# Kernel tuning notes

Hardware: AMD Instinct MI355X
Metric: run time of the kernel (lower is better)

## Reference

```python
import jax, jax.numpy as jnp
import numpy as np

N_CYCLES = 20000  # number of cycles in the cycle basis (segments)


def setup_inputs() -> dict:
    key = jax.random.key(0)
    k1, k2, k3, k4, k5 = jax.random.split(key, 5)
    B, NB, E = 256, 50000, 160000  # batch, n_branches, total cycle-basis entries
    c = jax.random.normal(k1, (B, NB), dtype=jnp.float32)
    s = jax.random.normal(k2, (B, NB), dtype=jnp.float32)
    # signs are +/-1
    cysigns = jnp.where(jax.random.uniform(k4, (E,)) < 0.5, -1.0, 1.0).astype(jnp.float32)
    cyinds = jax.random.randint(k3, (E,), 0, NB, dtype=jnp.int32)
    # from_value_rowids requires nondecreasing row ids
    cyrows = jnp.sort(jax.random.randint(k5, (E,), 0, N_CYCLES, dtype=jnp.int32))
    return {"c": c, "s": s, "cysigns": cysigns, "cyinds": cyinds, "cyrows": cyrows}


def reference(c, s, cysigns, cyinds, cyrows):
    # gather branch vars per cycle-basis entry: [B, E]
    cg = jnp.take(c, cyinds, axis=1)
    sg = cysigns * jnp.take(s, cyinds, axis=1)
    # tf.math.angle(tf.complex(rc, rs)) == atan2(imag, real)
    ang = jnp.arctan2(sg, cg)  # [B, E]
    # ragged per-cycle sum == segment_sum over the entry axis -> [N_CYCLES, B]
    v_kvl = jax.ops.segment_sum(ang.T, cyrows, num_segments=N_CYCLES)
    # scalar KVL violation
    return jnp.mean(jnp.abs(v_kvl))
```

## Files before the change

### kernel.cpp

```cpp
#include <hip/hip_runtime.h>

#define NB     50000
#define NB4    12500
#define BATCH  256
#define NCYC   20000
#define QSCALE  (127.0f / 3.14159265358979f)
#define DQSCALE (3.14159265358979f / 127.0f)

__device__ __forceinline__ float fast_atan2f(float y, float x) {
    const float ax = __builtin_fabsf(x);
    const float ay = __builtin_fabsf(y);
    const float mx = fmaxf(ax, ay);
    const float mn = fminf(ax, ay);
    const float t  = mn * __builtin_amdgcn_rcpf(mx);
    const float t2 = t * t;
    float p = fmaf(t2, fmaf(t2, fmaf(t2, fmaf(t2,
                  0.0208351f, -0.0851330f), 0.1801410f), -0.3302995f),
                  0.9998660f);
    p *= t;
    p = (ay > ax) ? (1.57079632679489662f - p) : p;
    p = (x < 0.0f) ? (3.14159265358979324f - p) : p;
    return copysignf(p, y);
}

__global__ __launch_bounds__(256) void theta_k(
        const float4* __restrict__ c4, const float4* __restrict__ s4,
        signed char* __restrict__ th) {
    __shared__ signed char t[64][68];
    const int u    = threadIdx.x;
    const int col4 = u & 15;
    const int brow = u >> 4;
    const int x4   = blockIdx.x * 16 + col4;
    const int bb   = blockIdx.y * 64;

    if (x4 < NB4) {
        #pragma unroll
        for (int j = 0; j < 4; ++j) {
            const int bl = brow + 16 * j;
            const float4 vc = c4[(size_t)(bb + bl) * NB4 + x4];
            const float4 vs = s4[(size_t)(bb + bl) * NB4 + x4];
            char4 q;
            q.x = (signed char)__float2int_rn(fast_atan2f(vs.x, vc.x) * QSCALE);
            q.y = (signed char)__float2int_rn(fast_atan2f(vs.y, vc.y) * QSCALE);
            q.z = (signed char)__float2int_rn(fast_atan2f(vs.z, vc.z) * QSCALE);
            q.w = (signed char)__float2int_rn(fast_atan2f(vs.w, vc.w) * QSCALE);
            *reinterpret_cast<char4*>(&t[bl][4 * col4]) = q;
        }
    }
    __syncthreads();
    const int g   = u & 15;
    const int nb0 = u >> 4;
    #pragma unroll
    for (int j = 0; j < 4; ++j) {
        const int nbl = nb0 + 16 * j;
        const int nb  = blockIdx.x * 64 + nbl;
        if (nb < NB) {
            char4 v;
            v.x = t[4 * g + 0][nbl];
            v.y = t[4 * g + 1][nbl];
            v.z = t[4 * g + 2][nbl];
            v.w = t[4 * g + 3][nbl];
            *reinterpret_cast<char4*>(&th[(size_t)nb * BATCH + bb + 4 * g]) = v;
        }
    }
}

__global__ __launch_bounds__(256) void kvl_main_k(
        const signed char* __restrict__ th,
        const float* __restrict__ signs, const int* __restrict__ inds,
        const int* __restrict__ rows, int E,
        float* __restrict__ partials) {
    __shared__ int bnd[5];
    const int tid = threadIdx.x;
    const int r0  = blockIdx.x * 4;
    if (tid < 5) {
        const int target = r0 + tid;
        int lo = 0, hi = E;
        while (lo < hi) { const int m = (lo + hi) >> 1; if (rows[m] < target) lo = m + 1; else hi = m; }
        bnd[tid] = lo;
    }
    __syncthreads();
    const int wave  = tid >> 6;
    const int lane  = tid & 63;
    const int start = bnd[wave];
    const int end   = bnd[wave + 1];

    float a0 = 0.f, a1 = 0.f, a2 = 0.f, a3 = 0.f;
    int e = start;
    for (; e + 2 <= end; e += 2) {
        const int   i0 = inds[e],  i1 = inds[e + 1];
        const float g0 = signs[e] * DQSCALE, g1 = signs[e + 1] * DQSCALE;
        const unsigned int u0 = *reinterpret_cast<const unsigned int*>(&th[(size_t)i0 * BATCH + lane * 4]);
        const unsigned int u1 = *reinterpret_cast<const unsigned int*>(&th[(size_t)i1 * BATCH + lane * 4]);
        a0 += g0 * (float)(signed char)(u0      ) + g1 * (float)(signed char)(u1      );
        a1 += g0 * (float)(signed char)(u0 >>  8) + g1 * (float)(signed char)(u1 >>  8);
        a2 += g0 * (float)(signed char)(u0 >> 16) + g1 * (float)(signed char)(u1 >> 16);
        a3 += g0 * (float)(signed char)(u0 >> 24) + g1 * (float)(signed char)(u1 >> 24);
    }
    if (e < end) {
        const float g0 = signs[e] * DQSCALE;
        const unsigned int u0 = *reinterpret_cast<const unsigned int*>(&th[(size_t)inds[e] * BATCH + lane * 4]);
        a0 += g0 * (float)(signed char)(u0      );
        a1 += g0 * (float)(signed char)(u0 >>  8);
        a2 += g0 * (float)(signed char)(u0 >> 16);
        a3 += g0 * (float)(signed char)(u0 >> 24);
    }
    float v = fabsf(a0) + fabsf(a1) + fabsf(a2) + fabsf(a3);
    #pragma unroll
    for (int off = 32; off > 0; off >>= 1)
        v += __shfl_down(v, off, 64);
    if (lane == 0) partials[r0 + wave] = v;
}

__global__ __launch_bounds__(1024) void reduce_k(
        const float* __restrict__ partials, float* __restrict__ out) {
    const int tid = threadIdx.x;
    float v = 0.f;
    for (int i = tid; i < NCYC; i += 1024) v += partials[i];
    #pragma unroll
    for (int off = 32; off > 0; off >>= 1)
        v += __shfl_down(v, off, 64);
    __shared__ float wsum[16];
    if ((tid & 63) == 0) wsum[tid >> 6] = v;
    __syncthreads();
    if (tid == 0) {
        float t = 0.f;
        #pragma unroll
        for (int w = 0; w < 16; ++w) t += wsum[w];
        out[0] = t * (1.0f / ((float)NCYC * (float)BATCH));
    }
}

__global__ void zero_out_k(float* out) { if (threadIdx.x == 0) out[0] = 0.0f; }

__global__ __launch_bounds__(256) void kvl_fallback_k(
        const float* __restrict__ c, const float* __restrict__ s,
        const float* __restrict__ signs, const int* __restrict__ inds,
        const int* __restrict__ rows, int E, float* __restrict__ out) {
    const int r = blockIdx.x;
    int lo = 0, hi = E;
    while (lo < hi) { const int m = (lo + hi) >> 1; if (rows[m] < r) lo = m + 1; else hi = m; }
    const int start = lo;
    hi = E;
    while (lo < hi) { const int m = (lo + hi) >> 1; if (rows[m] <= r) lo = m + 1; else hi = m; }
    const int end = lo;
    const int tid = threadIdx.x;
    float acc = 0.f;
    for (int e = start; e < end; ++e) {
        const int idx = inds[e];
        const float sg = signs[e];
        acc += atan2f(sg * s[(size_t)tid * NB + idx], c[(size_t)tid * NB + idx]);
    }
    float v = fabsf(acc);
    #pragma unroll
    for (int off = 32; off > 0; off >>= 1)
        v += __shfl_down(v, off, 64);
    __shared__ float wsum[4];
    if ((tid & 63) == 0) wsum[tid >> 6] = v;
    __syncthreads();
    if (tid == 0)
        atomicAdd(out, (wsum[0] + wsum[1] + wsum[2] + wsum[3]) *
                       (1.0f / ((float)NCYC * (float)BATCH)));
}

extern "C" void kernel_launch(void* const* d_in, const int* in_sizes, int n_in,
                              void* d_out, int out_size, void* d_ws, size_t ws_size,
                              hipStream_t stream) {
    const float* c       = (const float*)d_in[0];
    const float* s       = (const float*)d_in[1];
    const float* cysigns = (const float*)d_in[2];
    const int*   cyinds  = (const int*)d_in[3];
    const int*   cyrows  = (const int*)d_in[4];
    const int    E       = in_sizes[2];
    float* out = (float*)d_out;

    const size_t th_bytes = (size_t)NB * BATCH;
    const size_t need = th_bytes + (size_t)NCYC * sizeof(float);
    if (ws_size >= need) {
        signed char* th = (signed char*)d_ws;
        float* partials = (float*)(th + th_bytes);

        dim3 tg((NB4 + 15) / 16, BATCH / 64);
        theta_k<<<tg, 256, 0, stream>>>((const float4*)c, (const float4*)s, th);
        kvl_main_k<<<NCYC / 4, 256, 0, stream>>>(th, cysigns, cyinds, cyrows, E, partials);
        reduce_k<<<1, 1024, 0, stream>>>(partials, out);
    } else {
        zero_out_k<<<1, 64, 0, stream>>>(out);
        kvl_fallback_k<<<NCYC, 256, 0, stream>>>(c, s, cysigns, cyinds, cyrows, E, out);
    }
}
```

Baseline: 166.2 us.

## Fuse theta, KVL gather and reduction into one cooperative kernel with grid sync

Merges the three kernels (theta quantize/transpose, per-cycle gather-sum, final reduce) into one cooperative launch of 782 blocks that uses a grid-wide sync between phases. Row boundaries are precomputed once per cycle into a workspace array, so the per-block binary searches go away. The final reduction becomes a per-block atomicAdd. This removes two launch gaps, but it caps the grid at 782 blocks, so each block handles four batch tiles in the theta phase, and it adds the cost of the grid barrier.

```diff
diff --git a/kernel.cpp b/kernel.cpp
--- a/kernel.cpp
+++ b/kernel.cpp
@@ -1,11 +1,16 @@
 #include <hip/hip_runtime.h>
+#include <hip/hip_cooperative_groups.h>
+
+namespace cg = cooperative_groups;
 
 #define NB     50000
 #define NB4    12500
 #define BATCH  256
 #define NCYC   20000
+#define GRID_F 782
 #define QSCALE  (127.0f / 3.14159265358979f)
 #define DQSCALE (3.14159265358979f / 127.0f)
+#define OUTSCALE (1.0f / ((float)NCYC * (float)BATCH))
 
 __device__ __forceinline__ float fast_atan2f(float y, float x) {
     const float ax = __builtin_fabsf(x);
@@ -23,112 +28,103 @@
     return copysignf(p, y);
 }
 
-__global__ __launch_bounds__(256) void theta_k(
+__global__ __launch_bounds__(256, 4) void fused_k(
         const float4* __restrict__ c4, const float4* __restrict__ s4,
-        signed char* __restrict__ th) {
+        signed char* __restrict__ th, int* __restrict__ row_start,
+        const float* __restrict__ signs, const int* __restrict__ inds,
+        const int* __restrict__ rows, int E, float* __restrict__ out) {
     __shared__ signed char t[64][68];
-    const int u    = threadIdx.x;
+    __shared__ float wsum[4];
+    const int u = threadIdx.x;
+
+    if (blockIdx.x == 0 && u == 0) out[0] = 0.0f;
+
+    {
+        const int g = blockIdx.x * 256 + u;
+        if (g <= NCYC) {
+            int lo = 0, hi = E;
+            while (lo < hi) { const int m = (lo + hi) >> 1; if (rows[m] < g) lo = m + 1; else hi = m; }
+            row_start[g] = lo;
+        }
+    }
+
     const int col4 = u & 15;
     const int brow = u >> 4;
     const int x4   = blockIdx.x * 16 + col4;
-    const int bb   = blockIdx.y * 64;
-
-    if (x4 < NB4) {
+    #pragma unroll
+    for (int by = 0; by < 4; ++by) {
+        const int bb = by * 64;
+        if (x4 < NB4) {
+            #pragma unroll
+            for (int j = 0; j < 4; ++j) {
+                const int bl = brow + 16 * j;
+                const float4 vc = c4[(size_t)(bb + bl) * NB4 + x4];
+                const float4 vs = s4[(size_t)(bb + bl) * NB4 + x4];
+                char4 q;
+                q.x = (signed char)__float2int_rn(fast_atan2f(vs.x, vc.x) * QSCALE);
+                q.y = (signed char)__float2int_rn(fast_atan2f(vs.y, vc.y) * QSCALE);
+                q.z = (signed char)__float2int_rn(fast_atan2f(vs.z, vc.z) * QSCALE);
+                q.w = (signed char)__float2int_rn(fast_atan2f(vs.w, vc.w) * QSCALE);
+                *reinterpret_cast<char4*>(&t[bl][4 * col4]) = q;
+            }
+        }
+        __syncthreads();
+        const int g2  = u & 15;
+        const int nb0 = u >> 4;
         #pragma unroll
         for (int j = 0; j < 4; ++j) {
-            const int bl = brow + 16 * j;
-            const float4 vc = c4[(size_t)(bb + bl) * NB4 + x4];
-            const float4 vs = s4[(size_t)(bb + bl) * NB4 + x4];
-            char4 q;
-            q.x = (signed char)__float2int_rn(fast_atan2f(vs.x, vc.x) * QSCALE);
-            q.y = (signed char)__float2int_rn(fast_atan2f(vs.y, vc.y) * QSCALE);
-            q.z = (signed char)__float2int_rn(fast_atan2f(vs.z, vc.z) * QSCALE);
-            q.w = (signed char)__float2int_rn(fast_atan2f(vs.w, vc.w) * QSCALE);
-            *reinterpret_cast<char4*>(&t[bl][4 * col4]) = q;
+            const int nbl = nb0 + 16 * j;
+            const int nb  = blockIdx.x * 64 + nbl;
+            if (nb < NB) {
+                char4 v;
+                v.x = t[4 * g2 + 0][nbl];
+                v.y = t[4 * g2 + 1][nbl];
+                v.z = t[4 * g2 + 2][nbl];
+                v.w = t[4 * g2 + 3][nbl];
+                *reinterpret_cast<char4*>(&th[(size_t)nb * BATCH + bb + 4 * g2]) = v;
+            }
         }
+        __syncthreads();
     }
-    __syncthreads();
-    const int g   = u & 15;
-    const int nb0 = u >> 4;
-    #pragma unroll
-    for (int j = 0; j < 4; ++j) {
-        const int nbl = nb0 + 16 * j;
-        const int nb  = blockIdx.x * 64 + nbl;
-        if (nb < NB) {
-            char4 v;
-            v.x = t[4 * g + 0][nbl];
-            v.y = t[4 * g + 1][nbl];
-            v.z = t[4 * g + 2][nbl];
-            v.w = t[4 * g + 3][nbl];
-            *reinterpret_cast<char4*>(&th[(size_t)nb * BATCH + bb + 4 * g]) = v;
+
+    cg::this_grid().sync();
+
+    const int wave = u >> 6;
+    const int lane = u & 63;
+    const int w0   = blockIdx.x * 4 + wave;
+    float acc = 0.f;
+    for (int r = w0; r < NCYC; r += 4 * GRID_F) {
+        const int start = row_start[r];
+        const int end   = row_start[r + 1];
+        float a0 = 0.f, a1 = 0.f, a2 = 0.f, a3 = 0.f;
+        int e = start;
+        for (; e + 2 <= end; e += 2) {
+            const int   i0 = inds[e],  i1 = inds[e + 1];
+            const float g0 = signs[e] * DQSCALE, g1 = signs[e + 1] * DQSCALE;
+            const unsigned int u0 = *reinterpret_cast<const unsigned int*>(&th[(size_t)i0 * BATCH + lane * 4]);
+            const unsigned int u1 = *reinterpret_cast<const unsigned int*>(&th[(size_t)i1 * BATCH + lane * 4]);
+            a0 += g0 * (float)(signed char)(u0      ) + g1 * (float)(signed char)(u1      );
+            a1 += g0 * (float)(signed char)(u0 >>  8) + g1 * (float)(signed char)(u1 >>  8);
+            a2 += g0 * (float)(signed char)(u0 >> 16) + g1 * (float)(signed char)(u1 >> 16);
+            a3 += g0 * (float)(signed char)(u0 >> 24) + g1 * (float)(signed char)(u1 >> 24);
         }
+        if (e < end) {
+            const float g0 = signs[e] * DQSCALE;
+            const unsigned int u0 = *reinterpret_cast<const unsigned int*>(&th[(size_t)inds[e] * BATCH + lane * 4]);
+            a0 += g0 * (float)(signed char)(u0      );
+            a1 += g0 * (float)(signed char)(u0 >>  8);
+            a2 += g0 * (float)(signed char)(u0 >> 16);
+            a3 += g0 * (float)(signed char)(u0 >> 24);
+        }
+        acc += fabsf(a0) + fabsf(a1) + fabsf(a2) + fabsf(a3);
     }
-}
-
-__global__ __launch_bounds__(256) void kvl_main_k(
-        const signed char* __restrict__ th,
-        const float* __restrict__ signs, const int* __restrict__ inds,
-        const int* __restrict__ rows, int E,
-        float* __restrict__ partials) {
-    __shared__ int bnd[5];
-    const int tid = threadIdx.x;
-    const int r0  = blockIdx.x * 4;
-    if (tid < 5) {
-        const int target = r0 + tid;
-        int lo = 0, hi = E;
-        while (lo < hi) { const int m = (lo + hi) >> 1; if (rows[m] < target) lo = m + 1; else hi = m; }
-        bnd[tid] = lo;
-    }
-    __syncthreads();
-    const int wave  = tid >> 6;
-    const int lane  = tid & 63;
-    const int start = bnd[wave];
-    const int end   = bnd[wave + 1];
-
-    float a0 = 0.f, a1 = 0.f, a2 = 0.f, a3 = 0.f;
-    int e = start;
-    for (; e + 2 <= end; e += 2) {
-        const int   i0 = inds[e],  i1 = inds[e + 1];
-        const float g0 = signs[e] * DQSCALE, g1 = signs[e + 1] * DQSCALE;
-        const unsigned int u0 = *reinterpret_cast<const unsigned int*>(&th[(size_t)i0 * BATCH + lane * 4]);
-        const unsigned int u1 = *reinterpret_cast<const unsigned int*>(&th[(size_t)i1 * BATCH + lane * 4]);
-        a0 += g0 * (float)(signed char)(u0      ) + g1 * (float)(signed char)(u1      );
-        a1 += g0 * (float)(signed char)(u0 >>  8) + g1 * (float)(signed char)(u1 >>  8);
-        a2 += g0 * (float)(signed char)(u0 >> 16) + g1 * (float)(signed char)(u1 >> 16);
-        a3 += g0 * (float)(signed char)(u0 >> 24) + g1 * (float)(signed char)(u1 >> 24);
-    }
-    if (e < end) {
-        const float g0 = signs[e] * DQSCALE;
-        const unsigned int u0 = *reinterpret_cast<const unsigned int*>(&th[(size_t)inds[e] * BATCH + lane * 4]);
-        a0 += g0 * (float)(signed char)(u0      );
-        a1 += g0 * (float)(signed char)(u0 >>  8);
-        a2 += g0 * (float)(signed char)(u0 >> 16);
-        a3 += g0 * (float)(signed char)(u0 >> 24);
-    }
-    float v = fabsf(a0) + fabsf(a1) + fabsf(a2) + fabsf(a3);
     #pragma unroll
     for (int off = 32; off > 0; off >>= 1)
-        v += __shfl_down(v, off, 64);
-    if (lane == 0) partials[r0 + wave] = v;
-}
-
-__global__ __launch_bounds__(1024) void reduce_k(
-        const float* __restrict__ partials, float* __restrict__ out) {
-    const int tid = threadIdx.x;
-    float v = 0.f;
-    for (int i = tid; i < NCYC; i += 1024) v += partials[i];
-    #pragma unroll
-    for (int off = 32; off > 0; off >>= 1)
-        v += __shfl_down(v, off, 64);
-    __shared__ float wsum[16];
-    if ((tid & 63) == 0) wsum[tid >> 6] = v;
+        acc += __shfl_down(acc, off, 64);
+    if (lane == 0) wsum[wave] = acc;
     __syncthreads();
-    if (tid == 0) {
-        float t = 0.f;
-        #pragma unroll
-        for (int w = 0; w < 16; ++w) t += wsum[w];
-        out[0] = t * (1.0f / ((float)NCYC * (float)BATCH));
-    }
+    if (u == 0)
+        atomicAdd(out, (wsum[0] + wsum[1] + wsum[2] + wsum[3]) * OUTSCALE);
 }
 
 __global__ void zero_out_k(float* out) { if (threadIdx.x == 0) out[0] = 0.0f; }
@@ -171,19 +167,22 @@
     const float* cysigns = (const float*)d_in[2];
     const int*   cyinds  = (const int*)d_in[3];
     const int*   cyrows  = (const int*)d_in[4];
-    const int    E       = in_sizes[2];
+    int          E       = in_sizes[2];
     float* out = (float*)d_out;
 
     const size_t th_bytes = (size_t)NB * BATCH;
-    const size_t need = th_bytes + (size_t)NCYC * sizeof(float);
+    const size_t need = th_bytes + (size_t)(NCYC + 1) * sizeof(int);
     if (ws_size >= need) {
         signed char* th = (signed char*)d_ws;
-        float* partials = (float*)(th + th_bytes);
+        int* row_start  = (int*)(th + th_bytes);
 
-        dim3 tg((NB4 + 15) / 16, BATCH / 64);
-        theta_k<<<tg, 256, 0, stream>>>((const float4*)c, (const float4*)s, th);
-        kvl_main_k<<<NCYC / 4, 256, 0, stream>>>(th, cysigns, cyinds, cyrows, E, partials);
-        reduce_k<<<1, 1024, 0, stream>>>(partials, out);
+        const float4* c4 = (const float4*)c;
+        const float4* s4 = (const float4*)s;
+        void* args[] = {(void*)&c4, (void*)&s4, (void*)&th, (void*)&row_start,
+                        (void*)&cysigns, (void*)&cyinds, (void*)&cyrows,
+                        (void*)&E, (void*)&out};
+        hipLaunchCooperativeKernel((void*)fused_k, dim3(GRID_F), dim3(256),
+                                   args, 0, stream);
     } else {
         zero_out_k<<<1, 64, 0, stream>>>(out);
         kvl_fallback_k<<<NCYC, 256, 0, stream>>>(c, s, cysigns, cyinds, cyrows, E, out);
```

Result: slower. 258.3 us (+55.4%).

## Fuse final reduction into KVL kernel and precompute row boundaries in theta kernel

Applied to the files above, without the earlier changes.

Moves the per-cycle binary searches for segment boundaries into the theta kernel, where the blockIdx.y==0 blocks write a row_start array. The KVL kernel now reads its boundaries directly and reduces to one partial per block. The last block to finish, found with an atomic ticket counter, does the final reduction, which removes the separate single-block reduce launch. This cuts one kernel launch and the serial tail, at the cost of extra work in some theta blocks and an atomic plus fences per block.

```diff
diff --git a/kernel.cpp b/kernel.cpp
--- a/kernel.cpp
+++ b/kernel.cpp
@@ -6,6 +6,7 @@
 #define NCYC   20000
 #define QSCALE  (127.0f / 3.14159265358979f)
 #define DQSCALE (3.14159265358979f / 127.0f)
+#define OUTSCALE (1.0f / ((float)NCYC * (float)BATCH))
 
 __device__ __forceinline__ float fast_atan2f(float y, float x) {
     const float ax = __builtin_fabsf(x);
@@ -25,9 +26,22 @@
 
 __global__ __launch_bounds__(256) void theta_k(
         const float4* __restrict__ c4, const float4* __restrict__ s4,
-        signed char* __restrict__ th) {
+        signed char* __restrict__ th, int* __restrict__ row_start,
+        const int* __restrict__ rows, int E, int* __restrict__ counter) {
     __shared__ signed char t[64][68];
-    const int u    = threadIdx.x;
+    const int u = threadIdx.x;
+
+    if (blockIdx.x == 0 && blockIdx.y == 0 && u == 0) *counter = 0;
+
+    if (blockIdx.y == 0) {
+        const int g = blockIdx.x * 256 + u;
+        if (g <= NCYC) {
+            int lo = 0, hi = E;
+            while (lo < hi) { const int m = (lo + hi) >> 1; if (rows[m] < g) lo = m + 1; else hi = m; }
+            row_start[g] = lo;
+        }
+    }
+
     const int col4 = u & 15;
     const int brow = u >> 4;
     const int x4   = blockIdx.x * 16 + col4;
@@ -65,25 +79,20 @@
     }
 }
 
-__global__ __launch_bounds__(256) void kvl_main_k(
+__global__ __launch_bounds__(256) void kvl2_k(
         const signed char* __restrict__ th,
         const float* __restrict__ signs, const int* __restrict__ inds,
-        const int* __restrict__ rows, int E,
-        float* __restrict__ partials) {
-    __shared__ int bnd[5];
-    const int tid = threadIdx.x;
-    const int r0  = blockIdx.x * 4;
-    if (tid < 5) {
-        const int target = r0 + tid;
-        int lo = 0, hi = E;
-        while (lo < hi) { const int m = (lo + hi) >> 1; if (rows[m] < target) lo = m + 1; else hi = m; }
-        bnd[tid] = lo;
-    }
-    __syncthreads();
-    const int wave  = tid >> 6;
-    const int lane  = tid & 63;
-    const int start = bnd[wave];
-    const int end   = bnd[wave + 1];
+        const int* __restrict__ row_start,
+        float* __restrict__ partials, int* __restrict__ counter,
+        float* __restrict__ out) {
+    __shared__ float wsum[4];
+    __shared__ int   lastflag;
+    const int tid  = threadIdx.x;
+    const int wave = tid >> 6;
+    const int lane = tid & 63;
+    const int r    = blockIdx.x * 4 + wave;
+    const int start = row_start[r];
+    const int end   = row_start[r + 1];
 
     float a0 = 0.f, a1 = 0.f, a2 = 0.f, a3 = 0.f;
     int e = start;
@@ -109,25 +118,28 @@
     #pragma unroll
     for (int off = 32; off > 0; off >>= 1)
         v += __shfl_down(v, off, 64);
-    if (lane == 0) partials[r0 + wave] = v;
-}
-
-__global__ __launch_bounds__(1024) void reduce_k(
-        const float* __restrict__ partials, float* __restrict__ out) {
-    const int tid = threadIdx.x;
-    float v = 0.f;
-    for (int i = tid; i < NCYC; i += 1024) v += partials[i];
-    #pragma unroll
-    for (int off = 32; off > 0; off >>= 1)
-        v += __shfl_down(v, off, 64);
-    __shared__ float wsum[16];
-    if ((tid & 63) == 0) wsum[tid >> 6] = v;
-    __syncthreads();
+    if (lane == 0) wsum[wave] = v;
+    __syncthreads();
+
     if (tid == 0) {
-        float t = 0.f;
+        partials[blockIdx.x] = wsum[0] + wsum[1] + wsum[2] + wsum[3];
+        __threadfence();
+        const int ticket = atomicAdd(counter, 1);
+        lastflag = (ticket == gridDim.x - 1) ? 1 : 0;
+    }
+    __syncthreads();
+
+    if (lastflag) {
+        __threadfence();
+        float acc = 0.f;
+        for (int i = tid; i < (int)gridDim.x; i += 256) acc += partials[i];
         #pragma unroll
-        for (int w = 0; w < 16; ++w) t += wsum[w];
-        out[0] = t * (1.0f / ((float)NCYC * (float)BATCH));
+        for (int off = 32; off > 0; off >>= 1)
+            acc += __shfl_down(acc, off, 64);
+        if (lane == 0) wsum[wave] = acc;
+        __syncthreads();
+        if (tid == 0)
+            out[0] = (wsum[0] + wsum[1] + wsum[2] + wsum[3]) * OUTSCALE;
     }
 }
 
@@ -175,15 +187,20 @@
     float* out = (float*)d_out;
 
     const size_t th_bytes = (size_t)NB * BATCH;
-    const size_t need = th_bytes + (size_t)NCYC * sizeof(float);
+    const size_t rs_bytes = (size_t)(NCYC + 1) * sizeof(int);
+    const size_t pa_bytes = (size_t)(NCYC / 4) * sizeof(float);
+    const size_t need = th_bytes + rs_bytes + pa_bytes + sizeof(int);
     if (ws_size >= need) {
-        signed char* th = (signed char*)d_ws;
-        float* partials = (float*)(th + th_bytes);
+        signed char* th   = (signed char*)d_ws;
+        int* row_start    = (int*)(th + th_bytes);
+        float* partials   = (float*)((char*)row_start + rs_bytes);
+        int* counter      = (int*)((char*)partials + pa_bytes);
 
         dim3 tg((NB4 + 15) / 16, BATCH / 64);
-        theta_k<<<tg, 256, 0, stream>>>((const float4*)c, (const float4*)s, th);
-        kvl_main_k<<<NCYC / 4, 256, 0, stream>>>(th, cysigns, cyinds, cyrows, E, partials);
-        reduce_k<<<1, 1024, 0, stream>>>(partials, out);
+        theta_k<<<tg, 256, 0, stream>>>((const float4*)c, (const float4*)s,
+                                        th, row_start, cyrows, E, counter);
+        kvl2_k<<<NCYC / 4, 256, 0, stream>>>(th, cysigns, cyinds, row_start,
+                                             partials, counter, out);
     } else {
         zero_out_k<<<1, 64, 0, stream>>>(out);
         kvl_fallback_k<<<NCYC, 256, 0, stream>>>(c, s, cysigns, cyinds, cyrows, E, out);
```

New measurement: 255.4 us. 53.7% more time.
